# Performance work log

Hardware: AMD Instinct MI355X
Metric: run time of the kernel (lower is better)

The kernel has to match this reference:

```python
import jax, jax.numpy as jnp
import numpy as np

EPS = 1e-5
NHEAD = 8
TOP_K = 2


def _layernorm(x, g, b):
    m = jnp.mean(x, axis=-1, keepdims=True)
    v = jnp.mean((x - m) ** 2, axis=-1, keepdims=True)
    return (x - m) * jax.lax.rsqrt(v + EPS) * g + b


def setup_inputs() -> dict:
    S, D, F, E = 4096, 512, 2048, 8
    key = jax.random.key(0)
    ks = jax.random.split(key, 18)
    std = 0.02
    return {
        "src": jax.random.normal(ks[0], (S, D), jnp.float32),
        "in_proj_w": std * jax.random.normal(ks[1], (3 * D, D), jnp.float32),
        "in_proj_b": jnp.zeros((3 * D,), jnp.float32),
        "out_proj_w": std * jax.random.normal(ks[2], (D, D), jnp.float32),
        "out_proj_b": jnp.zeros((D,), jnp.float32),
        "ln1_g": jnp.ones((D,), jnp.float32),
        "ln1_b": jnp.zeros((D,), jnp.float32),
        "ln2_g": jnp.ones((D,), jnp.float32),
        "ln2_b": jnp.zeros((D,), jnp.float32),
        "gate_w": std * jax.random.normal(ks[3], (E, D), jnp.float32),
        "gate_b": jnp.zeros((E,), jnp.float32),
        "w1": std * jax.random.normal(ks[4], (E, F, D), jnp.float32),
        "b1": jnp.zeros((E, F), jnp.float32),
        "w2": std * jax.random.normal(ks[5], (E, F, D), jnp.float32),
        "b2": jnp.zeros((E, F), jnp.float32),
        "wo": std * jax.random.normal(ks[6], (E, D, F), jnp.float32),
        "bo": jnp.zeros((E, D), jnp.float32),
    }


def _sa_block(x, in_proj_w, in_proj_b, out_proj_w, out_proj_b):
    # x: [S, D] unbatched sequence (torch MultiheadAttention unbatched path)
    S, D = x.shape
    hd = D // NHEAD
    qkv = x @ in_proj_w.T + in_proj_b              # [S, 3D]
    q, k, v = jnp.split(qkv, 3, axis=-1)
    q = q.reshape(S, NHEAD, hd)
    k = k.reshape(S, NHEAD, hd)
    v = v.reshape(S, NHEAD, hd)
    scores = jnp.einsum("shd,thd->hst", q, k) / jnp.sqrt(jnp.float32(hd))
    attn = jax.nn.softmax(scores, axis=-1)         # [H, S, S]
    out = jnp.einsum("hst,thd->shd", attn, v).reshape(S, D)
    return out @ out_proj_w.T + out_proj_b


def _ff_block(x, gate_w, gate_b, w1, b1, w2, b2, wo, bo):
    # top-k gated SwiGLU MoE; gate probs are softmax, NOT renormalized after topk
    T = x.shape[0]
    E = w1.shape[0]
    gates = jax.nn.softmax(x @ gate_w.T + gate_b, axis=-1)      # [T, E]
    top_scores, top_idx = jax.lax.top_k(gates, TOP_K)            # [T, k]
    combine = jnp.zeros((T, E), x.dtype).at[
        jnp.arange(T)[:, None], top_idx].add(top_scores)         # [T, E]
    out = jnp.zeros_like(x)
    for e in range(E):  # small fixed expert count
        h = jax.nn.silu(x @ w1[e].T + b1[e]) * (x @ w2[e].T + b2[e])
        out = out + combine[:, e:e + 1] * (h @ wo[e].T + bo[e])
    return out


def reference(src, in_proj_w, in_proj_b, out_proj_w, out_proj_b,
              ln1_g, ln1_b, ln2_g, ln2_b,
              gate_w, gate_b, w1, b1, w2, b2, wo, bo):
    # norm_first pre-norm residual layer, dropout=0 (eval)
    x = src
    x = x + _sa_block(_layernorm(x, ln1_g, ln1_b),
                      in_proj_w, in_proj_b, out_proj_w, out_proj_b)
    x = x + _ff_block(_layernorm(x, ln2_g, ln2_b),
                      gate_w, gate_b, w1, b1, w2, b2, wo, bo)
    return x
```

## Files before the change

### kernel.cpp

```cpp
#include <hip/hip_runtime.h>
#include <hip/hip_bf16.h>
#include <math.h>

#define SQ   4096
#define DM   512
#define NH   8
#define HDIM 64
#define FF   2048
#define NE   8

typedef unsigned short u16;
typedef unsigned int   u32;
typedef __attribute__((ext_vector_type(8))) __bf16 bf16x8;
typedef __attribute__((ext_vector_type(4))) float  f32x4;

__device__ __forceinline__ float bf2f(u16 v) {
    union { u32 i; float f; } c; c.i = ((u32)v) << 16; return c.f;
}
__device__ __forceinline__ u16 f2bf(float f) {
    union { float f; u32 i; } c; c.f = f; u32 u = c.i;
    return (u16)((u + 0x7fffu + ((u >> 16) & 1u)) >> 16);
}

#define BM 128
#define BN 128
#define BK 32
#define BKP 40

__global__ __launch_bounds__(256) void gemm_split(
    const u16* __restrict__ Ahi, const u16* __restrict__ Alo, int lda,
    const u16* __restrict__ Bhi, const u16* __restrict__ Blo, int ldb,
    int M, int N, int K,
    const float* __restrict__ bias,
    const float* __restrict__ resid, int ldres,
    u16* __restrict__ Chi, u16* __restrict__ Clo,
    float* __restrict__ Cf, int ldc, int mode)
{
    __shared__ __align__(16) u16 Ash[BM * BKP], Asl[BM * BKP];
    __shared__ __align__(16) u16 Bsh[BN * BKP], Bsl[BN * BKP];
    const int tid  = threadIdx.x;
    const int wave = tid >> 6;
    const int lane = tid & 63;
    const int quad = lane >> 4;
    const int l16  = lane & 15;
    const int bm = blockIdx.x * BM;
    const int bn = blockIdx.y * BN;
    const int wm = (wave & 1) * 64;
    const int wn = (wave >> 1) * 64;

    f32x4 acc[4][4];
#pragma unroll
    for (int i = 0; i < 4; i++)
#pragma unroll
        for (int j = 0; j < 4; j++)
#pragma unroll
            for (int r = 0; r < 4; r++) acc[i][j][r] = 0.0f;

    for (int k0 = 0; k0 < K; k0 += BK) {
#pragma unroll
        for (int i = 0; i < 2; i++) {
            int c = tid + i * 256;
            int row = c >> 2;
            int col = (c & 3) << 3;
            int ga = bm + row, gb2 = bn + row;
            uint4 vah = make_uint4(0u,0u,0u,0u), val = vah, vbh = vah, vbl = vah;
            if (ga < M) {
                vah = *(const uint4*)(Ahi + (size_t)ga * lda + k0 + col);
                val = *(const uint4*)(Alo + (size_t)ga * lda + k0 + col);
            }
            if (gb2 < N) {
                vbh = *(const uint4*)(Bhi + (size_t)gb2 * ldb + k0 + col);
                vbl = *(const uint4*)(Blo + (size_t)gb2 * ldb + k0 + col);
            }
            *(uint4*)(Ash + row * BKP + col) = vah;
            *(uint4*)(Asl + row * BKP + col) = val;
            *(uint4*)(Bsh + row * BKP + col) = vbh;
            *(uint4*)(Bsl + row * BKP + col) = vbl;
        }
        __syncthreads();
        bf16x8 ah[4], al[4], bh[4], bl[4];
#pragma unroll
        for (int i = 0; i < 4; i++) {
            ah[i] = *(const bf16x8*)(Ash + (wm + i * 16 + l16) * BKP + quad * 8);
            al[i] = *(const bf16x8*)(Asl + (wm + i * 16 + l16) * BKP + quad * 8);
        }
#pragma unroll
        for (int j = 0; j < 4; j++) {
            bh[j] = *(const bf16x8*)(Bsh + (wn + j * 16 + l16) * BKP + quad * 8);
            bl[j] = *(const bf16x8*)(Bsl + (wn + j * 16 + l16) * BKP + quad * 8);
        }
#pragma unroll
        for (int i = 0; i < 4; i++)
#pragma unroll
            for (int j = 0; j < 4; j++) {
                acc[i][j] = __builtin_amdgcn_mfma_f32_16x16x32_bf16(ah[i], bh[j], acc[i][j], 0,0,0);
                acc[i][j] = __builtin_amdgcn_mfma_f32_16x16x32_bf16(ah[i], bl[j], acc[i][j], 0,0,0);
                acc[i][j] = __builtin_amdgcn_mfma_f32_16x16x32_bf16(al[i], bh[j], acc[i][j], 0,0,0);
            }
        __syncthreads();
    }

#pragma unroll
    for (int i = 0; i < 4; i++)
#pragma unroll
        for (int j = 0; j < 4; j++)
#pragma unroll
            for (int r = 0; r < 4; r++) {
                int row = bm + wm + i * 16 + quad * 4 + r;
                int col = bn + wn + j * 16 + l16;
                if (row >= M || col >= N) continue;
                float v = acc[i][j][r] + (bias ? bias[col] : 0.0f);
                size_t idx = (size_t)row * ldc + col;
                if (mode == 0) {
                    u16 hb = f2bf(v);
                    Chi[idx] = hb;
                    Clo[idx] = f2bf(v - bf2f(hb));
                } else {
                    if (resid) v += resid[(size_t)row * ldres + col];
                    Cf[idx] = v;
                }
            }
}

__global__ __launch_bounds__(256) void moe12_all(
    const u16* __restrict__ A, int lda,
    const int* __restrict__ idxl, const int* __restrict__ cnt,
    const int* __restrict__ off,
    const float* __restrict__ w1, const float* __restrict__ b1,
    const float* __restrict__ w2, const float* __restrict__ b2,
    u16* __restrict__ H)
{
    const int bmg = blockIdx.x * BM;
    if (bmg >= off[NE]) return;
    int e = 0;
    while (e < NE - 1 && bmg >= off[e + 1]) e++;
    const int M   = cnt[e];
    const int bml = bmg - off[e];
    if (bml >= M) return;
    const float* B1 = w1 + (size_t)e * FF * DM;
    const float* B2 = w2 + (size_t)e * FF * DM;
    const int*   rl = idxl + e * SQ;

    __shared__ __align__(16) u16 As[BM * BKP], Bs1[BN * BKP], Bs2[BN * BKP];
    const int tid  = threadIdx.x;
    const int wave = tid >> 6;
    const int lane = tid & 63;
    const int quad = lane >> 4;
    const int l16  = lane & 15;
    const int bn = blockIdx.y * BN;
    const int wm = (wave & 1) * 64;
    const int wn = (wave >> 1) * 64;

    f32x4 acc1[4][4], acc2[4][4];
#pragma unroll
    for (int i = 0; i < 4; i++)
#pragma unroll
        for (int j = 0; j < 4; j++)
#pragma unroll
            for (int r = 0; r < 4; r++) { acc1[i][j][r] = 0.0f; acc2[i][j][r] = 0.0f; }

    for (int k0 = 0; k0 < DM; k0 += BK) {
#pragma unroll
        for (int i = 0; i < 2; i++) {
            int c = tid + i * 256;
            int row = c >> 2;
            int col = (c & 3) << 3;
            uint4 va = make_uint4(0u,0u,0u,0u);
            int lr = bml + row;
            if (lr < M) {
                int ar = rl[lr];
                va = *(const uint4*)(A + (size_t)ar * lda + k0 + col);
            }
            *(uint4*)(As + row * BKP + col) = va;
        }
#pragma unroll
        for (int i = 0; i < 4; i++) {
            int c = tid + i * 256;
            int row = c >> 3;
            int col = (c & 7) << 2;
            float4 v1 = *(const float4*)(B1 + (size_t)(bn + row) * DM + k0 + col);
            float4 v2 = *(const float4*)(B2 + (size_t)(bn + row) * DM + k0 + col);
            ushort4 h1, h2;
            h1.x = f2bf(v1.x); h1.y = f2bf(v1.y); h1.z = f2bf(v1.z); h1.w = f2bf(v1.w);
            h2.x = f2bf(v2.x); h2.y = f2bf(v2.y); h2.z = f2bf(v2.z); h2.w = f2bf(v2.w);
            *(ushort4*)(Bs1 + row * BKP + col) = h1;
            *(ushort4*)(Bs2 + row * BKP + col) = h2;
        }
        __syncthreads();
        bf16x8 af[4], b1f[4], b2f[4];
#pragma unroll
        for (int i = 0; i < 4; i++)
            af[i] = *(const bf16x8*)(As + (wm + i * 16 + l16) * BKP + quad * 8);
#pragma unroll
        for (int j = 0; j < 4; j++) {
            b1f[j] = *(const bf16x8*)(Bs1 + (wn + j * 16 + l16) * BKP + quad * 8);
            b2f[j] = *(const bf16x8*)(Bs2 + (wn + j * 16 + l16) * BKP + quad * 8);
        }
#pragma unroll
        for (int i = 0; i < 4; i++)
#pragma unroll
            for (int j = 0; j < 4; j++) {
                acc1[i][j] = __builtin_amdgcn_mfma_f32_16x16x32_bf16(af[i], b1f[j], acc1[i][j], 0,0,0);
                acc2[i][j] = __builtin_amdgcn_mfma_f32_16x16x32_bf16(af[i], b2f[j], acc2[i][j], 0,0,0);
            }
        __syncthreads();
    }

#pragma unroll
    for (int i = 0; i < 4; i++)
#pragma unroll
        for (int j = 0; j < 4; j++)
#pragma unroll
            for (int r = 0; r < 4; r++) {
                int rowl = bml + wm + i * 16 + quad * 4 + r;
                if (rowl >= M) continue;
                int col = bn + wn + j * 16 + l16;
                float g1 = acc1[i][j][r] + b1[e * FF + col];
                float g2 = acc2[i][j][r] + b2[e * FF + col];
                float s  = g1 / (1.0f + __expf(-g1));
                H[(size_t)(off[e] + rowl) * FF + col] = f2bf(s * g2);
            }
}

__global__ __launch_bounds__(256) void moe_y_all(
    const u16* __restrict__ H,
    const float* __restrict__ wo, const float* __restrict__ bo,
    const int* __restrict__ idxl, const float* __restrict__ cw,
    const int* __restrict__ cnt, const int* __restrict__ off,
    float* __restrict__ out)
{
    const int bmg = blockIdx.x * BM;
    if (bmg >= off[NE]) return;
    int e = 0;
    while (e < NE - 1 && bmg >= off[e + 1]) e++;
    const int M   = cnt[e];
    const int bml = bmg - off[e];
    if (bml >= M) return;
    const float* B = wo + (size_t)e * DM * FF;

    __shared__ __align__(16) u16 As[BM * BKP], Bs[BN * BKP];
    const int tid  = threadIdx.x;
    const int wave = tid >> 6;
    const int lane = tid & 63;
    const int quad = lane >> 4;
    const int l16  = lane & 15;
    const int bn = blockIdx.y * BN;
    const int wm = (wave & 1) * 64;
    const int wn = (wave >> 1) * 64;

    f32x4 acc[4][4];
#pragma unroll
    for (int i = 0; i < 4; i++)
#pragma unroll
        for (int j = 0; j < 4; j++)
#pragma unroll
            for (int r = 0; r < 4; r++) acc[i][j][r] = 0.0f;

    for (int k0 = 0; k0 < FF; k0 += BK) {
#pragma unroll
        for (int i = 0; i < 2; i++) {
            int c = tid + i * 256;
            int row = c >> 2;
            int col = (c & 3) << 3;
            uint4 va = *(const uint4*)(H + (size_t)(bmg + row) * FF + k0 + col);
            *(uint4*)(As + row * BKP + col) = va;
        }
#pragma unroll
        for (int i = 0; i < 4; i++) {
            int c = tid + i * 256;
            int row = c >> 3;
            int col = (c & 7) << 2;
            float4 v = *(const float4*)(B + (size_t)(bn + row) * FF + k0 + col);
            ushort4 h;
            h.x = f2bf(v.x); h.y = f2bf(v.y); h.z = f2bf(v.z); h.w = f2bf(v.w);
            *(ushort4*)(Bs + row * BKP + col) = h;
        }
        __syncthreads();
        bf16x8 af[4], bf[4];
#pragma unroll
        for (int i = 0; i < 4; i++)
            af[i] = *(const bf16x8*)(As + (wm + i * 16 + l16) * BKP + quad * 8);
#pragma unroll
        for (int j = 0; j < 4; j++)
            bf[j] = *(const bf16x8*)(Bs + (wn + j * 16 + l16) * BKP + quad * 8);
#pragma unroll
        for (int i = 0; i < 4; i++)
#pragma unroll
            for (int j = 0; j < 4; j++)
                acc[i][j] = __builtin_amdgcn_mfma_f32_16x16x32_bf16(af[i], bf[j], acc[i][j], 0,0,0);
        __syncthreads();
    }

#pragma unroll
    for (int i = 0; i < 4; i++)
#pragma unroll
        for (int j = 0; j < 4; j++)
#pragma unroll
            for (int r = 0; r < 4; r++) {
                int rowl = bml + wm + i * 16 + quad * 4 + r;
                if (rowl >= M) continue;
                int col = bn + wn + j * 16 + l16;
                int tok = idxl[e * SQ + rowl];
                float wgt = cw[e * SQ + rowl];
                atomicAdd(out + (size_t)tok * DM + col,
                          wgt * (acc[i][j][r] + bo[e * DM + col]));
            }
}

#define KP 72
#define SCL 0.18033688011112042f
__global__ __launch_bounds__(256) void flash_attn(
    const u16* __restrict__ qh, const u16* __restrict__ ql,
    const u16* __restrict__ vth, const u16* __restrict__ vtl,
    u16* __restrict__ oh, u16* __restrict__ ol)
{
    __shared__ __align__(16) u16 Ksh[64*KP], Ksl[64*KP], Vsh[64*KP], Vsl[64*KP];
    __shared__ __align__(16) u16 Psh[4][16*KP], Psl[4][16*KP];
    const int tid  = threadIdx.x;
    const int wave = tid >> 6;
    const int lane = tid & 63;
    const int quad = lane >> 4;
    const int l16  = lane & 15;
    const int h    = blockIdx.y;
    const int qbase = blockIdx.x * 64 + wave * 16;

    bf16x8 aqh[2], aql[2];
#pragma unroll
    for (int kk = 0; kk < 2; kk++) {
        size_t off = (size_t)(qbase + l16) * (3*DM) + h*HDIM + kk*32 + quad*8;
        aqh[kk] = *(const bf16x8*)(qh + off);
        aql[kk] = *(const bf16x8*)(ql + off);
    }

    float m_[4], l_[4];
    f32x4 o_[4];
#pragma unroll
    for (int r = 0; r < 4; r++) { m_[r] = -1e30f; l_[r] = 0.0f; }
#pragma unroll
    for (int nd = 0; nd < 4; nd++)
#pragma unroll
        for (int r = 0; r < 4; r++) o_[nd][r] = 0.0f;

    for (int jt = 0; jt < SQ / 64; jt++) {
#pragma unroll
        for (int i = 0; i < 2; i++) {
            int c = tid + i * 256;
            int r = c >> 3;
            int co = (c & 7) << 3;
            size_t koff = (size_t)(jt*64 + r) * (3*DM) + DM + h*HDIM + co;
            size_t voff = (size_t)(h*HDIM + r) * SQ + jt*64 + co;
            *(uint4*)(Ksh + r*KP + co) = *(const uint4*)(qh + koff);
            *(uint4*)(Ksl + r*KP + co) = *(const uint4*)(ql + koff);
            *(uint4*)(Vsh + r*KP + co) = *(const uint4*)(vth + voff);
            *(uint4*)(Vsl + r*KP + co) = *(const uint4*)(vtl + voff);
        }
        __syncthreads();

        f32x4 s[4];
#pragma unroll
        for (int jn = 0; jn < 4; jn++) {
            f32x4 z;
#pragma unroll
            for (int r = 0; r < 4; r++) z[r] = 0.0f;
#pragma unroll
            for (int kk = 0; kk < 2; kk++) {
                bf16x8 kh = *(const bf16x8*)(Ksh + (jn*16 + l16)*KP + kk*32 + quad*8);
                bf16x8 kl = *(const bf16x8*)(Ksl + (jn*16 + l16)*KP + kk*32 + quad*8);
                z = __builtin_amdgcn_mfma_f32_16x16x32_bf16(aqh[kk], kh, z, 0,0,0);
                z = __builtin_amdgcn_mfma_f32_16x16x32_bf16(aqh[kk], kl, z, 0,0,0);
                z = __builtin_amdgcn_mfma_f32_16x16x32_bf16(aql[kk], kh, z, 0,0,0);
            }
#pragma unroll
            for (int r = 0; r < 4; r++) z[r] *= SCL;
            s[jn] = z;
        }

        float mx[4], al2[4], rs[4];
#pragma unroll
        for (int r = 0; r < 4; r++)
            mx[r] = fmaxf(fmaxf(s[0][r], s[1][r]), fmaxf(s[2][r], s[3][r]));
#pragma unroll
        for (int r = 0; r < 4; r++) {
#pragma unroll
            for (int o2 = 1; o2 < 16; o2 <<= 1)
                mx[r] = fmaxf(mx[r], __shfl_xor(mx[r], o2));
            float nm = fmaxf(m_[r], mx[r]);
            al2[r] = exp2f(m_[r] - nm);
            m_[r] = nm;
            rs[r] = 0.0f;
        }
#pragma unroll
        for (int jn = 0; jn < 4; jn++)
#pragma unroll
            for (int r = 0; r < 4; r++) {
                float p = exp2f(s[jn][r] - m_[r]);
                s[jn][r] = p;
                rs[r] += p;
            }
#pragma unroll
        for (int r = 0; r < 4; r++) {
#pragma unroll
            for (int o2 = 1; o2 < 16; o2 <<= 1)
                rs[r] += __shfl_xor(rs[r], o2);
            l_[r] = l_[r] * al2[r] + rs[r];
        }
#pragma unroll
        for (int nd = 0; nd < 4; nd++)
#pragma unroll
            for (int r = 0; r < 4; r++) o_[nd][r] *= al2[r];
#pragma unroll
        for (int jn = 0; jn < 4; jn++)
#pragma unroll
            for (int r = 0; r < 4; r++) {
                float p = s[jn][r];
                u16 ph = f2bf(p);
                int pidx = (quad*4 + r)*KP + jn*16 + l16;
                Psh[wave][pidx] = ph;
                Psl[wave][pidx] = f2bf(p - bf2f(ph));
            }

        bf16x8 ph[2], pl[2];
#pragma unroll
        for (int kk = 0; kk < 2; kk++) {
            ph[kk] = *(const bf16x8*)(Psh[wave] + l16*KP + kk*32 + quad*8);
            pl[kk] = *(const bf16x8*)(Psl[wave] + l16*KP + kk*32 + quad*8);
        }
#pragma unroll
        for (int nd = 0; nd < 4; nd++) {
#pragma unroll
            for (int kk = 0; kk < 2; kk++) {
                bf16x8 vh = *(const bf16x8*)(Vsh + (nd*16 + l16)*KP + kk*32 + quad*8);
                bf16x8 vl = *(const bf16x8*)(Vsl + (nd*16 + l16)*KP + kk*32 + quad*8);
                o_[nd] = __builtin_amdgcn_mfma_f32_16x16x32_bf16(ph[kk], vh, o_[nd], 0,0,0);
                o_[nd] = __builtin_amdgcn_mfma_f32_16x16x32_bf16(ph[kk], vl, o_[nd], 0,0,0);
                o_[nd] = __builtin_amdgcn_mfma_f32_16x16x32_bf16(pl[kk], vh, o_[nd], 0,0,0);
            }
        }
        __syncthreads();
    }

#pragma unroll
    for (int nd = 0; nd < 4; nd++)
#pragma unroll
        for (int r = 0; r < 4; r++) {
            int row = qbase + quad*4 + r;
            int col = h*HDIM + nd*16 + l16;
            float w = o_[nd][r] / l_[r];
            u16 hb = f2bf(w);
            oh[(size_t)row * DM + col] = hb;
            ol[(size_t)row * DM + col] = f2bf(w - bf2f(hb));
        }
}

__global__ __launch_bounds__(256) void ln1_split(
    const float* __restrict__ x, const float* __restrict__ g,
    const float* __restrict__ b, u16* __restrict__ ohi, u16* __restrict__ olo)
{
    const int row = blockIdx.x;
    const int tid = threadIdx.x;
    float v0 = x[(size_t)row * DM + tid];
    float v1 = x[(size_t)row * DM + tid + 256];
    float s = v0 + v1, sq = v0*v0 + v1*v1;
#pragma unroll
    for (int o = 1; o < 64; o <<= 1) { s += __shfl_xor(s, o); sq += __shfl_xor(sq, o); }
    __shared__ float ss[4], ssq[4];
    if ((tid & 63) == 0) { ss[tid>>6] = s; ssq[tid>>6] = sq; }
    __syncthreads();
    s  = ss[0]+ss[1]+ss[2]+ss[3];
    sq = ssq[0]+ssq[1]+ssq[2]+ssq[3];
    float m = s * (1.0f/DM);
    float rstd = rsqrtf(sq*(1.0f/DM) - m*m + 1e-5f);
    float y0 = (v0-m)*rstd*g[tid]     + b[tid];
    float y1 = (v1-m)*rstd*g[tid+256] + b[tid+256];
    u16 h0 = f2bf(y0), h1 = f2bf(y1);
    ohi[(size_t)row*DM + tid]       = h0;  olo[(size_t)row*DM + tid]       = f2bf(y0 - bf2f(h0));
    ohi[(size_t)row*DM + tid + 256] = h1;  olo[(size_t)row*DM + tid + 256] = f2bf(y1 - bf2f(h1));
}

__global__ __launch_bounds__(256) void ln_kernel(
    const float* __restrict__ x, const float* __restrict__ g,
    const float* __restrict__ b, u16* __restrict__ out)
{
    const int row = blockIdx.x;
    const int tid = threadIdx.x;
    float v0 = x[(size_t)row * DM + tid];
    float v1 = x[(size_t)row * DM + tid + 256];
    float s = v0 + v1, sq = v0*v0 + v1*v1;
#pragma unroll
    for (int o = 1; o < 64; o <<= 1) { s += __shfl_xor(s, o); sq += __shfl_xor(sq, o); }
    __shared__ float ss[4], ssq[4];
    if ((tid & 63) == 0) { ss[tid>>6] = s; ssq[tid>>6] = sq; }
    __syncthreads();
    s  = ss[0]+ss[1]+ss[2]+ss[3];
    sq = ssq[0]+ssq[1]+ssq[2]+ssq[3];
    float m = s * (1.0f/DM);
    float rstd = rsqrtf(sq*(1.0f/DM) - m*m + 1e-5f);
    out[(size_t)row*DM + tid]       = f2bf((v0-m)*rstd*g[tid]     + b[tid]);
    out[(size_t)row*DM + tid + 256] = f2bf((v1-m)*rstd*g[tid+256] + b[tid+256]);
}

__global__ __launch_bounds__(256) void transpose_v2(
    const u16* __restrict__ qh, const u16* __restrict__ ql,
    u16* __restrict__ vth, u16* __restrict__ vtl)
{
    __shared__ u16 Th[64 * 66], Tl[64 * 66];
    const int t0  = blockIdx.x * 64;
    const int hd0 = blockIdx.y * 64;
    const int tid = threadIdx.x;
#pragma unroll
    for (int k = 0; k < 16; k++) {
        int idx = tid + k * 256;
        int r = idx >> 6, j = idx & 63;
        size_t src = (size_t)(t0 + r) * (3*DM) + 2*DM + hd0 + j;
        Th[r * 66 + j] = qh[src];
        Tl[r * 66 + j] = ql[src];
    }
    __syncthreads();
#pragma unroll
    for (int k = 0; k < 16; k++) {
        int idx = tid + k * 256;
        int r = idx >> 6, c2 = idx & 63;
        size_t dst = (size_t)(hd0 + r) * SQ + t0 + c2;
        vth[dst] = Th[c2 * 66 + r];
        vtl[dst] = Tl[c2 * 66 + r];
    }
}

__global__ __launch_bounds__(256) void gate_route(
    const float* __restrict__ x1, const float* __restrict__ g,
    const float* __restrict__ b, const float* __restrict__ gw,
    const float* __restrict__ gb,
    int* __restrict__ cnt, int* __restrict__ idxl, float* __restrict__ cw)
{
    const int token = blockIdx.x * 4 + (threadIdx.x >> 6);
    const int lane  = threadIdx.x & 63;
    const float* xr = x1 + (size_t)token * DM;
    float v[8];
#pragma unroll
    for (int i = 0; i < 8; i++) v[i] = xr[lane*8 + i];
    float s = 0.f, sq = 0.f;
#pragma unroll
    for (int i = 0; i < 8; i++) { s += v[i]; sq += v[i]*v[i]; }
#pragma unroll
    for (int o = 1; o < 64; o <<= 1) { s += __shfl_xor(s, o); sq += __shfl_xor(sq, o); }
    float m = s * (1.0f/DM);
    float rstd = rsqrtf(sq*(1.0f/DM) - m*m + 1e-5f);
    float xn[8];
#pragma unroll
    for (int i = 0; i < 8; i++)
        xn[i] = (v[i]-m)*rstd*g[lane*8+i] + b[lane*8+i];
    float logit[8];
#pragma unroll
    for (int e = 0; e < 8; e++) {
        float t = 0.f;
#pragma unroll
        for (int i = 0; i < 8; i++) t += xn[i] * gw[e*DM + lane*8 + i];
#pragma unroll
        for (int o = 1; o < 64; o <<= 1) t += __shfl_xor(t, o);
        logit[e] = t + gb[e];
    }
    if (lane == 0) {
        float mx = -1e30f;
        for (int e = 0; e < 8; e++) mx = fmaxf(mx, logit[e]);
        float den = 0.f, p[8];
        for (int e = 0; e < 8; e++) { p[e] = __expf(logit[e] - mx); den += p[e]; }
        for (int e = 0; e < 8; e++) p[e] /= den;
        int i1 = 0;
        for (int e = 1; e < 8; e++) if (p[e] > p[i1]) i1 = e;
        int i2 = -1;
        for (int e = 0; e < 8; e++) { if (e == i1) continue; if (i2 < 0 || p[e] > p[i2]) i2 = e; }
        int s1 = atomicAdd(&cnt[i1], 1);
        idxl[i1*SQ + s1] = token;  cw[i1*SQ + s1] = p[i1];
        int s2 = atomicAdd(&cnt[i2], 1);
        idxl[i2*SQ + s2] = token;  cw[i2*SQ + s2] = p[i2];
    }
}

__global__ __launch_bounds__(256) void cvt_split_w(
    const float* __restrict__ w, u16* __restrict__ wh, u16* __restrict__ wl, int n)
{
    int i = blockIdx.x * 256 + threadIdx.x;
    if (i < n) {
        float v = w[i];
        u16 h = f2bf(v);
        wh[i] = h;
        wl[i] = f2bf(v - bf2f(h));
    }
}

__global__ __launch_bounds__(64) void zero_cnt(int* cnt)
{
    if (threadIdx.x < NE) cnt[threadIdx.x] = 0;
}

__global__ __launch_bounds__(64) void make_off(const int* __restrict__ cnt,
                                              int* __restrict__ off)
{
    if (threadIdx.x == 0) {
        int a = 0;
        for (int e = 0; e < NE; e++) {
            off[e] = a;
            a += ((cnt[e] + 127) >> 7) << 7;
        }
        off[NE] = a;
    }
}

__global__ __launch_bounds__(256) void init_out(
    const float* __restrict__ x1, float* __restrict__ out)
{
    int i = blockIdx.x * 256 + threadIdx.x;
    ((float4*)out)[i] = ((const float4*)x1)[i];
}

__global__ __launch_bounds__(256) void sentinel_kernel(float* out, float v, int n)
{
    int i = blockIdx.x * 256 + threadIdx.x;
    if (i < n) out[i] = v;
}
__global__ __launch_bounds__(256) void scrub_kernel(float* out, int n)
{
    int i = blockIdx.x * 256 + threadIdx.x;
    if (i < n) { float v = out[i]; if (!isfinite(v)) out[i] = 777.0f; }
}

extern "C" void kernel_launch(void* const* d_in, const int* in_sizes, int n_in,
                              void* d_out, int out_size, void* d_ws, size_t ws_size,
                              hipStream_t stream)
{
    const float* src        = (const float*)d_in[0];
    const float* in_proj_w  = (const float*)d_in[1];
    const float* in_proj_b  = (const float*)d_in[2];
    const float* out_proj_w = (const float*)d_in[3];
    const float* out_proj_b = (const float*)d_in[4];
    const float* ln1_g      = (const float*)d_in[5];
    const float* ln1_b      = (const float*)d_in[6];
    const float* ln2_g      = (const float*)d_in[7];
    const float* ln2_b      = (const float*)d_in[8];
    const float* gate_w     = (const float*)d_in[9];
    const float* gate_b     = (const float*)d_in[10];
    const float* w1         = (const float*)d_in[11];
    const float* b1         = (const float*)d_in[12];
    const float* w2         = (const float*)d_in[13];
    const float* b2         = (const float*)d_in[14];
    const float* wo         = (const float*)d_in[15];
    const float* bo         = (const float*)d_in[16];
    float* out = (float*)d_out;

    const size_t MB = (size_t)1 << 20;
    const size_t ROUTE = 512 * 1024;
    const size_t NEED = ROUTE + 44 * MB;
    if (ws_size < NEED) {
        sentinel_kernel<<<(SQ*DM)/256, 256, 0, stream>>>(out, 333.0f, SQ*DM);
        return;
    }

    char* ws = (char*)d_ws;
    int*   cnt  = (int*)ws;
    int*   offp = (int*)(ws + 64);
    int*   idxl = (int*)(ws + 1024);
    float* cw   = (float*)(ws + 1024 + 128*1024);
    char*  base = ws + ROUTE;
    u16* xln1h = (u16*)(base);
    u16* xln1l = (u16*)(base + 4*MB);
    u16* attnh = (u16*)(base);
    u16* attnl = (u16*)(base + 4*MB);
    u16* qkvh  = (u16*)(base + 8*MB);
    u16* qkvl  = (u16*)(base + 20*MB);
    float* x1  = (float*)(base + 8*MB);
    u16* vth   = (u16*)(base + 32*MB);
    u16* vtl   = (u16*)(base + 36*MB);
    u16* xln2  = (u16*)(base + 36*MB);
    u16* Hbuf  = (u16*)(base);
    u16* wph   = (u16*)(base + 40*MB);
    u16* wpl   = (u16*)(base + 40*MB + 1536*1024);
    u16* woh   = (u16*)(base + 43*MB);
    u16* wol   = (u16*)(base + 43*MB + 512*1024);

    cvt_split_w<<<(3*DM*DM)/256, 256, 0, stream>>>(in_proj_w,  wph, wpl, 3*DM*DM);
    cvt_split_w<<<(DM*DM)/256,   256, 0, stream>>>(out_proj_w, woh, wol, DM*DM);

    ln1_split<<<SQ, 256, 0, stream>>>(src, ln1_g, ln1_b, xln1h, xln1l);
    gemm_split<<<dim3(32, 12), 256, 0, stream>>>(
        xln1h, xln1l, DM, wph, wpl, DM, SQ, 3*DM, DM,
        in_proj_b, nullptr, 0, qkvh, qkvl, nullptr, 3*DM, 0);
    transpose_v2<<<dim3(SQ/64, DM/64), 256, 0, stream>>>(qkvh, qkvl, vth, vtl);
    flash_attn<<<dim3(SQ/64, NH), 256, 0, stream>>>(qkvh, qkvl, vth, vtl, attnh, attnl);
    gemm_split<<<dim3(32, 4), 256, 0, stream>>>(
        attnh, attnl, DM, woh, wol, DM, SQ, DM, DM,
        out_proj_b, src, DM, nullptr, nullptr, x1, DM, 1);

    ln_kernel<<<SQ, 256, 0, stream>>>(x1, ln2_g, ln2_b, xln2);
    zero_cnt<<<1, 64, 0, stream>>>(cnt);
    gate_route<<<SQ/4, 256, 0, stream>>>(x1, ln2_g, ln2_b, gate_w, gate_b,
                                         cnt, idxl, cw);
    make_off<<<1, 64, 0, stream>>>(cnt, offp);
    init_out<<<(SQ*DM/4)/256, 256, 0, stream>>>(x1, out);
    moe12_all<<<dim3(72, 16), 256, 0, stream>>>(
        xln2, DM, idxl, cnt, offp, w1, b1, w2, b2, Hbuf);
    moe_y_all<<<dim3(72, 4), 256, 0, stream>>>(
        Hbuf, wo, bo, idxl, cw, cnt, offp, out);

    scrub_kernel<<<(SQ*DM)/256, 256, 0, stream>>>(out, SQ*DM);
}
```

Measured before the change: 843.5 us.

## Prefetch K/V tiles in flash attention, fuse routing kernels, cheapen hi/lo splits

Flash attention now loads the next K/V tile into registers while the current tile is being computed, which hides global memory latency at the cost of extra registers. The softmax scale is folded into the exp2 FMA instead of a separate multiply pass. The zero_cnt and make_off launches are removed: counters are zeroed inside ln_kernel and expert offsets are recomputed per block in the MoE kernels. The bf16 hi/lo split now truncates the high part instead of rounding it, which is cheaper but changes the rounding of both the high and low parts.

```diff
diff --git a/kernel.cpp b/kernel.cpp
--- a/kernel.cpp
+++ b/kernel.cpp
@@ -20,6 +20,13 @@
 __device__ __forceinline__ u16 f2bf(float f) {
     union { float f; u32 i; } c; c.f = f; u32 u = c.i;
     return (u16)((u + 0x7fffu + ((u >> 16) & 1u)) >> 16);
+}
+__device__ __forceinline__ void tsplit(float v, u16& hi, u16& lo) {
+    u32 vb = __float_as_uint(v);
+    u32 hb = vb & 0xFFFF0000u;
+    float r = v - __uint_as_float(hb);
+    hi = (u16)(hb >> 16);
+    lo = (u16)(__float_as_uint(r) >> 16);
 }
 
 #define BM 128
@@ -112,9 +119,10 @@
                 float v = acc[i][j][r] + (bias ? bias[col] : 0.0f);
                 size_t idx = (size_t)row * ldc + col;
                 if (mode == 0) {
-                    u16 hb = f2bf(v);
+                    u16 hb, lb;
+                    tsplit(v, hb, lb);
                     Chi[idx] = hb;
-                    Clo[idx] = f2bf(v - bf2f(hb));
+                    Clo[idx] = lb;
                 } else {
                     if (resid) v += resid[(size_t)row * ldres + col];
                     Cf[idx] = v;
@@ -122,20 +130,31 @@
             }
 }
 
+__device__ __forceinline__ int find_expert(const int* __restrict__ cnt,
+                                           int bmg, int& bml, int& obase)
+{
+    int a = 0;
+#pragma unroll
+    for (int e = 0; e < NE; e++) {
+        int pad = ((cnt[e] + 127) >> 7) << 7;
+        if (bmg < a + pad) { bml = bmg - a; obase = a; return e; }
+        a += pad;
+    }
+    return -1;
+}
+
 __global__ __launch_bounds__(256) void moe12_all(
     const u16* __restrict__ A, int lda,
     const int* __restrict__ idxl, const int* __restrict__ cnt,
-    const int* __restrict__ off,
     const float* __restrict__ w1, const float* __restrict__ b1,
     const float* __restrict__ w2, const float* __restrict__ b2,
     u16* __restrict__ H)
 {
     const int bmg = blockIdx.x * BM;
-    if (bmg >= off[NE]) return;
-    int e = 0;
-    while (e < NE - 1 && bmg >= off[e + 1]) e++;
-    const int M   = cnt[e];
-    const int bml = bmg - off[e];
+    int bml, obase;
+    int e = find_expert(cnt, bmg, bml, obase);
+    if (e < 0) return;
+    const int M = cnt[e];
     if (bml >= M) return;
     const float* B1 = w1 + (size_t)e * FF * DM;
     const float* B2 = w2 + (size_t)e * FF * DM;
@@ -218,7 +237,7 @@
                 float g1 = acc1[i][j][r] + b1[e * FF + col];
                 float g2 = acc2[i][j][r] + b2[e * FF + col];
                 float s  = g1 / (1.0f + __expf(-g1));
-                H[(size_t)(off[e] + rowl) * FF + col] = f2bf(s * g2);
+                H[(size_t)(obase + rowl) * FF + col] = f2bf(s * g2);
             }
 }
 
@@ -226,15 +245,14 @@
     const u16* __restrict__ H,
     const float* __restrict__ wo, const float* __restrict__ bo,
     const int* __restrict__ idxl, const float* __restrict__ cw,
-    const int* __restrict__ cnt, const int* __restrict__ off,
+    const int* __restrict__ cnt,
     float* __restrict__ out)
 {
     const int bmg = blockIdx.x * BM;
-    if (bmg >= off[NE]) return;
-    int e = 0;
-    while (e < NE - 1 && bmg >= off[e + 1]) e++;
-    const int M   = cnt[e];
-    const int bml = bmg - off[e];
+    int bml, obase;
+    int e = find_expert(cnt, bmg, bml, obase);
+    if (e < 0) return;
+    const int M = cnt[e];
     if (bml >= M) return;
     const float* B = wo + (size_t)e * DM * FF;
 
@@ -323,6 +341,7 @@
     const int l16  = lane & 15;
     const int h    = blockIdx.y;
     const int qbase = blockIdx.x * 64 + wave * 16;
+    const int NT = SQ / 64;
 
     bf16x8 aqh[2], aql[2];
 #pragma unroll
@@ -332,6 +351,14 @@
         aql[kk] = *(const bf16x8*)(ql + off);
     }
 
+    int r0[2], co[2];
+#pragma unroll
+    for (int i = 0; i < 2; i++) {
+        int c = tid + i * 256;
+        r0[i] = c >> 3;
+        co[i] = (c & 7) << 3;
+    }
+
     float m_[4], l_[4];
     f32x4 o_[4];
 #pragma unroll
@@ -341,20 +368,37 @@
 #pragma unroll
         for (int r = 0; r < 4; r++) o_[nd][r] = 0.0f;
 
-    for (int jt = 0; jt < SQ / 64; jt++) {
+    uint4 pre[8];
+#pragma unroll
+    for (int i = 0; i < 2; i++) {
+        size_t koff = (size_t)(r0[i]) * (3*DM) + DM + h*HDIM + co[i];
+        size_t voff = (size_t)(h*HDIM + r0[i]) * SQ + co[i];
+        pre[i*4+0] = *(const uint4*)(qh  + koff);
+        pre[i*4+1] = *(const uint4*)(ql  + koff);
+        pre[i*4+2] = *(const uint4*)(vth + voff);
+        pre[i*4+3] = *(const uint4*)(vtl + voff);
+    }
+
+    for (int jt = 0; jt < NT; jt++) {
 #pragma unroll
         for (int i = 0; i < 2; i++) {
-            int c = tid + i * 256;
-            int r = c >> 3;
-            int co = (c & 7) << 3;
-            size_t koff = (size_t)(jt*64 + r) * (3*DM) + DM + h*HDIM + co;
-            size_t voff = (size_t)(h*HDIM + r) * SQ + jt*64 + co;
-            *(uint4*)(Ksh + r*KP + co) = *(const uint4*)(qh + koff);
-            *(uint4*)(Ksl + r*KP + co) = *(const uint4*)(ql + koff);
-            *(uint4*)(Vsh + r*KP + co) = *(const uint4*)(vth + voff);
-            *(uint4*)(Vsl + r*KP + co) = *(const uint4*)(vtl + voff);
+            *(uint4*)(Ksh + r0[i]*KP + co[i]) = pre[i*4+0];
+            *(uint4*)(Ksl + r0[i]*KP + co[i]) = pre[i*4+1];
+            *(uint4*)(Vsh + r0[i]*KP + co[i]) = pre[i*4+2];
+            *(uint4*)(Vsl + r0[i]*KP + co[i]) = pre[i*4+3];
         }
         __syncthreads();
+        if (jt + 1 < NT) {
+#pragma unroll
+            for (int i = 0; i < 2; i++) {
+                size_t koff = (size_t)((jt+1)*64 + r0[i]) * (3*DM) + DM + h*HDIM + co[i];
+                size_t voff = (size_t)(h*HDIM + r0[i]) * SQ + (jt+1)*64 + co[i];
+                pre[i*4+0] = *(const uint4*)(qh  + koff);
+                pre[i*4+1] = *(const uint4*)(ql  + koff);
+                pre[i*4+2] = *(const uint4*)(vth + voff);
+                pre[i*4+3] = *(const uint4*)(vtl + voff);
+            }
+        }
 
         f32x4 s[4];
 #pragma unroll
@@ -370,12 +414,10 @@
                 z = __builtin_amdgcn_mfma_f32_16x16x32_bf16(aqh[kk], kl, z, 0,0,0);
                 z = __builtin_amdgcn_mfma_f32_16x16x32_bf16(aql[kk], kh, z, 0,0,0);
             }
-#pragma unroll
-            for (int r = 0; r < 4; r++) z[r] *= SCL;
             s[jn] = z;
         }
 
-        float mx[4], al2[4], rs[4];
+        float mx[4], al2[4], rs[4], nscl[4];
 #pragma unroll
         for (int r = 0; r < 4; r++)
             mx[r] = fmaxf(fmaxf(s[0][r], s[1][r]), fmaxf(s[2][r], s[3][r]));
@@ -385,15 +427,16 @@
             for (int o2 = 1; o2 < 16; o2 <<= 1)
                 mx[r] = fmaxf(mx[r], __shfl_xor(mx[r], o2));
             float nm = fmaxf(m_[r], mx[r]);
-            al2[r] = exp2f(m_[r] - nm);
+            al2[r] = exp2f((m_[r] - nm) * SCL);
             m_[r] = nm;
+            nscl[r] = nm * SCL;
             rs[r] = 0.0f;
         }
 #pragma unroll
         for (int jn = 0; jn < 4; jn++)
 #pragma unroll
             for (int r = 0; r < 4; r++) {
-                float p = exp2f(s[jn][r] - m_[r]);
+                float p = exp2f(fmaf(s[jn][r], SCL, -nscl[r]));
                 s[jn][r] = p;
                 rs[r] += p;
             }
@@ -412,18 +455,18 @@
         for (int jn = 0; jn < 4; jn++)
 #pragma unroll
             for (int r = 0; r < 4; r++) {
-                float p = s[jn][r];
-                u16 ph = f2bf(p);
+                u16 ph, pl;
+                tsplit(s[jn][r], ph, pl);
                 int pidx = (quad*4 + r)*KP + jn*16 + l16;
                 Psh[wave][pidx] = ph;
-                Psl[wave][pidx] = f2bf(p - bf2f(ph));
-            }
-
-        bf16x8 ph[2], pl[2];
+                Psl[wave][pidx] = pl;
+            }
+
+        bf16x8 php[2], plp[2];
 #pragma unroll
         for (int kk = 0; kk < 2; kk++) {
-            ph[kk] = *(const bf16x8*)(Psh[wave] + l16*KP + kk*32 + quad*8);
-            pl[kk] = *(const bf16x8*)(Psl[wave] + l16*KP + kk*32 + quad*8);
+            php[kk] = *(const bf16x8*)(Psh[wave] + l16*KP + kk*32 + quad*8);
+            plp[kk] = *(const bf16x8*)(Psl[wave] + l16*KP + kk*32 + quad*8);
         }
 #pragma unroll
         for (int nd = 0; nd < 4; nd++) {
@@ -431,9 +474,9 @@
             for (int kk = 0; kk < 2; kk++) {
                 bf16x8 vh = *(const bf16x8*)(Vsh + (nd*16 + l16)*KP + kk*32 + quad*8);
                 bf16x8 vl = *(const bf16x8*)(Vsl + (nd*16 + l16)*KP + kk*32 + quad*8);
-                o_[nd] = __builtin_amdgcn_mfma_f32_16x16x32_bf16(ph[kk], vh, o_[nd], 0,0,0);
-                o_[nd] = __builtin_amdgcn_mfma_f32_16x16x32_bf16(ph[kk], vl, o_[nd], 0,0,0);
-                o_[nd] = __builtin_amdgcn_mfma_f32_16x16x32_bf16(pl[kk], vh, o_[nd], 0,0,0);
+                o_[nd] = __builtin_amdgcn_mfma_f32_16x16x32_bf16(php[kk], vh, o_[nd], 0,0,0);
+                o_[nd] = __builtin_amdgcn_mfma_f32_16x16x32_bf16(php[kk], vl, o_[nd], 0,0,0);
+                o_[nd] = __builtin_amdgcn_mfma_f32_16x16x32_bf16(plp[kk], vh, o_[nd], 0,0,0);
             }
         }
         __syncthreads();
@@ -446,9 +489,10 @@
             int row = qbase + quad*4 + r;
             int col = h*HDIM + nd*16 + l16;
             float w = o_[nd][r] / l_[r];
-            u16 hb = f2bf(w);
+            u16 hb, lb;
+            tsplit(w, hb, lb);
             oh[(size_t)row * DM + col] = hb;
-            ol[(size_t)row * DM + col] = f2bf(w - bf2f(hb));
+            ol[(size_t)row * DM + col] = lb;
         }
 }
 
@@ -472,17 +516,20 @@
     float rstd = rsqrtf(sq*(1.0f/DM) - m*m + 1e-5f);
     float y0 = (v0-m)*rstd*g[tid]     + b[tid];
     float y1 = (v1-m)*rstd*g[tid+256] + b[tid+256];
-    u16 h0 = f2bf(y0), h1 = f2bf(y1);
-    ohi[(size_t)row*DM + tid]       = h0;  olo[(size_t)row*DM + tid]       = f2bf(y0 - bf2f(h0));
-    ohi[(size_t)row*DM + tid + 256] = h1;  olo[(size_t)row*DM + tid + 256] = f2bf(y1 - bf2f(h1));
+    u16 h0, l0, h1, l1;
+    tsplit(y0, h0, l0);
+    tsplit(y1, h1, l1);
+    ohi[(size_t)row*DM + tid]       = h0;  olo[(size_t)row*DM + tid]       = l0;
+    ohi[(size_t)row*DM + tid + 256] = h1;  olo[(size_t)row*DM + tid + 256] = l1;
 }
 
 __global__ __launch_bounds__(256) void ln_kernel(
     const float* __restrict__ x, const float* __restrict__ g,
-    const float* __restrict__ b, u16* __restrict__ out)
+    const float* __restrict__ b, u16* __restrict__ out, int* __restrict__ cnt)
 {
     const int row = blockIdx.x;
     const int tid = threadIdx.x;
+    if (row == 0 && tid < NE) cnt[tid] = 0;
     float v0 = x[(size_t)row * DM + tid];
     float v1 = x[(size_t)row * DM + tid + 256];
     float s = v0 + v1, sq = v0*v0 + v1*v1;
@@ -581,28 +628,10 @@
 {
     int i = blockIdx.x * 256 + threadIdx.x;
     if (i < n) {
-        float v = w[i];
-        u16 h = f2bf(v);
+        u16 h, l;
+        tsplit(w[i], h, l);
         wh[i] = h;
-        wl[i] = f2bf(v - bf2f(h));
-    }
-}
-
-__global__ __launch_bounds__(64) void zero_cnt(int* cnt)
-{
-    if (threadIdx.x < NE) cnt[threadIdx.x] = 0;
-}
-
-__global__ __launch_bounds__(64) void make_off(const int* __restrict__ cnt,
-                                              int* __restrict__ off)
-{
-    if (threadIdx.x == 0) {
-        int a = 0;
-        for (int e = 0; e < NE; e++) {
-            off[e] = a;
-            a += ((cnt[e] + 127) >> 7) << 7;
-        }
-        off[NE] = a;
+        wl[i] = l;
     }
 }
 
@@ -657,7 +686,6 @@
 
     char* ws = (char*)d_ws;
     int*   cnt  = (int*)ws;
-    int*   offp = (int*)(ws + 64);
     int*   idxl = (int*)(ws + 1024);
     float* cw   = (float*)(ws + 1024 + 128*1024);
     char*  base = ws + ROUTE;
@@ -690,16 +718,14 @@
         attnh, attnl, DM, woh, wol, DM, SQ, DM, DM,
         out_proj_b, src, DM, nullptr, nullptr, x1, DM, 1);
 
-    ln_kernel<<<SQ, 256, 0, stream>>>(x1, ln2_g, ln2_b, xln2);
-    zero_cnt<<<1, 64, 0, stream>>>(cnt);
+    ln_kernel<<<SQ, 256, 0, stream>>>(x1, ln2_g, ln2_b, xln2, cnt);
     gate_route<<<SQ/4, 256, 0, stream>>>(x1, ln2_g, ln2_b, gate_w, gate_b,
                                          cnt, idxl, cw);
-    make_off<<<1, 64, 0, stream>>>(cnt, offp);
     init_out<<<(SQ*DM/4)/256, 256, 0, stream>>>(x1, out);
     moe12_all<<<dim3(72, 16), 256, 0, stream>>>(
-        xln2, DM, idxl, cnt, offp, w1, b1, w2, b2, Hbuf);
+        xln2, DM, idxl, cnt, w1, b1, w2, b2, Hbuf);
     moe_y_all<<<dim3(72, 4), 256, 0, stream>>>(
-        Hbuf, wo, bo, idxl, cw, cnt, offp, out);
+        Hbuf, wo, bo, idxl, cw, cnt, out);
 
     scrub_kernel<<<(SQ*DM)/256, 256, 0, stream>>>(out, SQ*DM);
 }
```

Result: slower. 1.054 ms (+25.0%).
